# Kernel tuning notes

Hardware: AMD Instinct MI355X
Metric: run time of the kernel (lower is better)

The kernel has to match this reference:

```python
import jax, jax.numpy as jnp
import numpy as np

B, N, D, H = 4, 4096, 512, 512
EDGE_P = 0.01  # adjacency density


def _glorot(key, shape):
    fan_in, fan_out = shape
    limit = np.sqrt(6.0 / (fan_in + fan_out)).astype(np.float32)
    return jax.random.uniform(key, shape, jnp.float32, -limit, limit)


def setup_inputs() -> dict:
    key = jax.random.key(0)
    ks = jax.random.split(key, 9)
    batch_graph = jax.random.normal(ks[0], (B, N, D), jnp.float32)
    adj = (jax.random.uniform(ks[1], (B, N, N)) < EDGE_P).astype(jnp.float32)
    adj = jnp.minimum(adj + jnp.eye(N, dtype=jnp.float32)[None], 1.0)  # self loops, 0/1
    return {
        "batch_graph": batch_graph,
        "adj": adj,
        "W1": _glorot(ks[2], (D, H)), "b1": jnp.zeros((H,), jnp.float32),
        "W2": _glorot(ks[3], (H, H)), "b2": jnp.zeros((H,), jnp.float32),
        "W3": _glorot(ks[4], (H, D)), "b3": jnp.zeros((D,), jnp.float32),
    }


def _normalize_adj(adj):
    # Faithful to GCN.normalize_sparse_adj: D^{-1/2} A^T D^{-1/2}
    rowsum = adj.sum(axis=1)                       # [B, N] (sum over dim 1, as in torch)
    d_inv_sqrt = jnp.where(rowsum > 0, jax.lax.rsqrt(jnp.maximum(rowsum, 1e-30)), 0.0)
    # (A @ diag(d))^T @ diag(d)  ->  d_i * A[j,i] * d_j
    return d_inv_sqrt[:, :, None] * jnp.swapaxes(adj, 1, 2) * d_inv_sqrt[:, None, :]


def reference(batch_graph, adj, W1, b1, W2, b2, W3, b3):
    # Block-diagonal big_adj @ big_graph == independent per-batch matmuls;
    # we exploit that instead of materializing the [B*N, B*N] dense matrix.
    a = _normalize_adj(adj)                                   # [B, N, N]
    # GraphConvolution (pygcn-style): out = adj @ (x @ W) + b; dropout = identity (eval)
    h = jax.nn.relu(jnp.einsum('bij,bjd->bid', a, batch_graph @ W1) + b1)
    h = jax.nn.relu(jnp.einsum('bij,bjd->bid', a, h @ W2) + b2)
    out = jnp.einsum('bij,bjd->bid', a, h @ W3) + b3          # [B, N, D]
    return out
```

## Files before the change

kernel.cpp:

```cpp
#include <hip/hip_runtime.h>
#include <stdint.h>

#define CAP 128
#define RPB 4

typedef __attribute__((ext_vector_type(8))) short bf16x8;
typedef __attribute__((ext_vector_type(4))) float f32x4;

typedef __attribute__((address_space(3))) uint32_t lds_u32;
typedef __attribute__((address_space(1))) const uint32_t glb_u32;

__device__ __forceinline__ unsigned short f2bf(float f) {
  union { float f; uint32_t u; } c; c.f = f;
  return (unsigned short)((c.u + 0x7fffu + ((c.u >> 16) & 1u)) >> 16);
}
__device__ __forceinline__ float bf2f(uint32_t b) {
  union { uint32_t u; float f; } c; c.u = b << 16; return c.f;
}
__device__ __forceinline__ float as_f32(uint32_t u) {
  union { uint32_t u; float f; } c; c.u = u; return c.f;
}

__global__ __launch_bounds__(256) void k_detect(const uint32_t* __restrict__ a,
                                                int* __restrict__ flag) {
  int i = blockIdx.x * 256 + threadIdx.x;
  bool found = false;
  for (int k = 0; k < 64; k++) {
    uint32_t x = a[(size_t)k * 65536 + i];
    if (x == 0x00003F80u || x == 0x3F803F80u) found = true;
  }
  if (found) flag[0] = 1;
}

__global__ __launch_bounds__(256) void k_build(const void* __restrict__ adjp,
                                               int* __restrict__ cnt,
                                               int* __restrict__ cols,
                                               const int* __restrict__ flag) {
  int gid = blockIdx.x * 256 + threadIdx.x;
  if (flag[0]) {
    const uint4* a = (const uint4*)adjp;
    uint4 v = a[gid];
    int i0 = (gid & 511) * 8;
    int j  = (gid >> 9) & 4095;
    int b  = gid >> 21;
    int base = b << 12;
    uint32_t w[4] = {v.x, v.y, v.z, v.w};
#pragma unroll
    for (int q = 0; q < 4; q++) {
      if (w[q] & 0xffffu) {
        int c = base + i0 + q * 2;
        int p = atomicAdd(&cnt[c], 1);
        if (p < CAP) cols[(size_t)c * CAP + p] = j;
      }
      if (w[q] >> 16) {
        int c = base + i0 + q * 2 + 1;
        int p = atomicAdd(&cnt[c], 1);
        if (p < CAP) cols[(size_t)c * CAP + p] = j;
      }
    }
  } else {
    const float4* a = (const float4*)adjp;
#pragma unroll
    for (int it = 0; it < 2; it++) {
      int v4 = gid + it * 8388608;
      float4 v = a[v4];
      int i0 = (v4 & 1023) * 4;
      int j  = (v4 >> 10) & 4095;
      int b  = v4 >> 22;
      int base = b << 12;
      float e[4] = {v.x, v.y, v.z, v.w};
#pragma unroll
      for (int q = 0; q < 4; q++) {
        if (e[q] != 0.0f) {
          int c = base + i0 + q;
          int p = atomicAdd(&cnt[c], 1);
          if (p < CAP) cols[(size_t)c * CAP + p] = j;
        }
      }
    }
  }
}

__global__ __launch_bounds__(256) void k_prep(const int* __restrict__ cnt,
                                              float* __restrict__ dinv,
                                              const void* b1, const void* b2,
                                              const void* b3,
                                              float* __restrict__ b1f,
                                              float* __restrict__ b2f,
                                              float* __restrict__ b3f,
                                              const int* __restrict__ flag) {
  int id = blockIdx.x * 256 + threadIdx.x;
  if (id < 16384) {
    int c = cnt[id];
    dinv[id] = (c > 0) ? 1.0f / sqrtf((float)c) : 0.0f;
  } else {
    int o = id - 16384;
    if (o < 1536) {
      const void* src = (o < 512) ? b1 : (o < 1024) ? b2 : b3;
      float* dst = (o < 512) ? b1f : (o < 1024) ? b2f : b3f;
      int i = o & 511;
      dst[i] = flag[0] ? bf2f(((const ushort*)src)[i]) : ((const float*)src)[i];
    }
  }
}

__global__ __launch_bounds__(256) void k_convx(const void* __restrict__ xp,
                                               ushort* __restrict__ xb,
                                               const int* __restrict__ flag) {
  int gid = blockIdx.x * 256 + threadIdx.x;
  if (flag[0]) {
    const uint4* in = (const uint4*)xp;
    ((uint4*)xb)[gid] = in[gid];
  } else {
    const float4* in = (const float4*)xp;
#pragma unroll
    for (int it = 0; it < 2; it++) {
      int i = gid + it * 1048576;
      float4 v = in[i];
      uint32_t lo = (uint32_t)f2bf(v.x) | ((uint32_t)f2bf(v.y) << 16);
      uint32_t hi = (uint32_t)f2bf(v.z) | ((uint32_t)f2bf(v.w) << 16);
      ((uint2*)xb)[i] = make_uint2(lo, hi);
    }
  }
}

__global__ __launch_bounds__(256) void k_wconv(const void* w1, const void* w2,
                                               const void* w3,
                                               ushort* __restrict__ wt1,
                                               ushort* __restrict__ wt2,
                                               ushort* __restrict__ wt3,
                                               const int* __restrict__ flag) {
  int id = blockIdx.x * 256 + threadIdx.x;
  int w = id >> 18;
  int o = id & 262143;
  const void* wp = (w == 0) ? w1 : (w == 1) ? w2 : w3;
  ushort* wt = (w == 0) ? wt1 : (w == 1) ? wt2 : wt3;
  int n = o >> 9, k = o & 511;
  if (flag[0]) wt[o] = ((const ushort*)wp)[k * 512 + n];
  else         wt[o] = f2bf(((const float*)wp)[k * 512 + n]);
}

__device__ __forceinline__ void gl_lds16(const ushort* g, ushort* l) {
  __builtin_amdgcn_global_load_lds((glb_u32*)g, (lds_u32*)l, 16, 0, 0);
}

__global__ __launch_bounds__(256) void k_gemm(const ushort* __restrict__ X,
                                              const ushort* __restrict__ WT,
                                              ushort* __restrict__ Z) {
  __shared__ ushort As[128 * 32];
  __shared__ ushort Bs[128 * 32];
  const int K = 512, NO = 512;
  int tid = threadIdx.x;
  int m0 = blockIdx.y * 128, n0 = blockIdx.x * 128;
  int lane = tid & 63;
  int wv = tid >> 6;
  int wm = (wv >> 1) << 6;
  int wn = (wv & 1) << 6;
  int lr = lane & 15;
  int lq = lane >> 4;

  f32x4 zero = {0.f, 0.f, 0.f, 0.f};
  f32x4 acc[4][4];
#pragma unroll
  for (int im = 0; im < 4; im++)
#pragma unroll
    for (int in_ = 0; in_ < 4; in_++) acc[im][in_] = zero;

  const ushort* Xg = X  + (size_t)(m0 + (tid >> 2)) * K + ((tid & 3) << 3);
  const ushort* Wg = WT + (size_t)(n0 + (tid >> 2)) * K + ((tid & 3) << 3);

  for (int kt = 0; kt < K; kt += 32) {
    __syncthreads();
    gl_lds16(Xg + kt,                    &As[tid * 8]);
    gl_lds16(Xg + kt + (size_t)64 * K,   &As[2048 + tid * 8]);
    gl_lds16(Wg + kt,                    &Bs[tid * 8]);
    gl_lds16(Wg + kt + (size_t)64 * K,   &Bs[2048 + tid * 8]);
    __syncthreads();
    bf16x8 af[4], bfr[4];
#pragma unroll
    for (int im = 0; im < 4; im++)
      af[im] = *(const bf16x8*)&As[(wm + im * 16 + lr) * 32 + lq * 8];
#pragma unroll
    for (int in_ = 0; in_ < 4; in_++)
      bfr[in_] = *(const bf16x8*)&Bs[(wn + in_ * 16 + lr) * 32 + lq * 8];
#pragma unroll
    for (int im = 0; im < 4; im++)
#pragma unroll
      for (int in_ = 0; in_ < 4; in_++)
        acc[im][in_] = __builtin_amdgcn_mfma_f32_16x16x32_bf16(
            af[im], bfr[in_], acc[im][in_], 0, 0, 0);
  }

#pragma unroll
  for (int im = 0; im < 4; im++) {
    int row0 = m0 + wm + im * 16 + lq * 4;
#pragma unroll
    for (int in_ = 0; in_ < 4; in_++) {
      int col = n0 + wn + in_ * 16 + lr;
#pragma unroll
      for (int r = 0; r < 4; r++)
        Z[(size_t)(row0 + r) * NO + col] = f2bf(acc[im][in_][r]);
    }
  }
}

__global__ __launch_bounds__(256) void k_spmm(const ushort* __restrict__ Z,
                                              const int* __restrict__ cnt,
                                              const int* __restrict__ cols,
                                              const float* __restrict__ dinv,
                                              const float* __restrict__ bias,
                                              void* __restrict__ outp,
                                              int do_relu, int is_final,
                                              const int* __restrict__ flag) {
  __shared__ int   sj[RPB][CAP];
  __shared__ float sv[RPB][CAP];
  int B = blockIdx.x;
  int wv = threadIdx.x >> 6;
  int lane = threadIdx.x & 63;
  int batch = (B & 7) >> 1;
  int lb = ((B >> 3) << 1) | (B & 1);
  int r = (batch << 12) + lb * RPB + wv;
  int base = batch << 12;

  int nnz = cnt[r];
  if (nnz > CAP) nnz = CAP;
  float dr = dinv[r];
  for (int k = lane; k < nnz; k += 64) {
    int j = cols[(size_t)r * CAP + k];
    sj[wv][k] = j;
    sv[wv][k] = dr * dinv[base + j];
  }

  const ushort* Zb = Z + (size_t)base * 512 + lane * 8;
  const float4* bp = (const float4*)bias + lane * 2;
  float4 bb0 = bp[0], bb1 = bp[1];
  float a[8] = {bb0.x, bb0.y, bb0.z, bb0.w, bb1.x, bb1.y, bb1.z, bb1.w};

  int k = 0;
  for (; k + 2 <= nnz; k += 2) {
    int j0 = sj[wv][k], j1 = sj[wv][k + 1];
    float v0 = sv[wv][k], v1 = sv[wv][k + 1];
    uint4 z0 = *(const uint4*)(Zb + (size_t)j0 * 512);
    uint4 z1 = *(const uint4*)(Zb + (size_t)j1 * 512);
    uint32_t w0[4] = {z0.x, z0.y, z0.z, z0.w};
    uint32_t w1[4] = {z1.x, z1.y, z1.z, z1.w};
#pragma unroll
    for (int q = 0; q < 4; q++) {
      a[q * 2]     += v0 * as_f32(w0[q] << 16);
      a[q * 2 + 1] += v0 * as_f32(w0[q] & 0xffff0000u);
      a[q * 2]     += v1 * as_f32(w1[q] << 16);
      a[q * 2 + 1] += v1 * as_f32(w1[q] & 0xffff0000u);
    }
  }
  if (k < nnz) {
    int j0 = sj[wv][k];
    float v0 = sv[wv][k];
    uint4 z0 = *(const uint4*)(Zb + (size_t)j0 * 512);
    uint32_t w0[4] = {z0.x, z0.y, z0.z, z0.w};
#pragma unroll
    for (int q = 0; q < 4; q++) {
      a[q * 2]     += v0 * as_f32(w0[q] << 16);
      a[q * 2 + 1] += v0 * as_f32(w0[q] & 0xffff0000u);
    }
  }

  if (do_relu) {
#pragma unroll
    for (int q = 0; q < 8; q++) a[q] = fmaxf(a[q], 0.f);
  }

  if (!is_final || flag[0]) {
    uint4 o;
    o.x = (uint32_t)f2bf(a[0]) | ((uint32_t)f2bf(a[1]) << 16);
    o.y = (uint32_t)f2bf(a[2]) | ((uint32_t)f2bf(a[3]) << 16);
    o.z = (uint32_t)f2bf(a[4]) | ((uint32_t)f2bf(a[5]) << 16);
    o.w = (uint32_t)f2bf(a[6]) | ((uint32_t)f2bf(a[7]) << 16);
    *(uint4*)((ushort*)outp + (size_t)r * 512 + lane * 8) = o;
  } else {
    float4 o0 = make_float4(a[0], a[1], a[2], a[3]);
    float4 o1 = make_float4(a[4], a[5], a[6], a[7]);
    float4* op = (float4*)((float*)outp + (size_t)r * 512 + lane * 8);
    op[0] = o0; op[1] = o1;
  }
}

extern "C" void kernel_launch(void* const* d_in, const int* in_sizes, int n_in,
                              void* d_out, int out_size, void* d_ws, size_t ws_size,
                              hipStream_t stream) {
  const void* X  = d_in[0];
  const void* A  = d_in[1];
  const void* W1 = d_in[2]; const void* b1 = d_in[3];
  const void* W2 = d_in[4]; const void* b2 = d_in[5];
  const void* W3 = d_in[6]; const void* b3 = d_in[7];

  char* ws = (char*)d_ws;
  size_t off = 0;
  auto alloc = [&](size_t bytes) -> void* {
    void* p = ws + off;
    off += (bytes + 255) & ~(size_t)255;
    return p;
  };
  int*    cnt  = (int*)alloc(16384 * 4);
  int*    flag = (int*)alloc(4);
  float*  dinv = (float*)alloc(16384 * 4);
  int*    cols = (int*)alloc((size_t)16384 * CAP * 4);
  ushort* W1T  = (ushort*)alloc(512 * 512 * 2);
  ushort* W2T  = (ushort*)alloc(512 * 512 * 2);
  ushort* W3T  = (ushort*)alloc(512 * 512 * 2);
  float*  b1f  = (float*)alloc(512 * 4);
  float*  b2f  = (float*)alloc(512 * 4);
  float*  b3f  = (float*)alloc(512 * 4);
  ushort* Xb   = (ushort*)alloc((size_t)16384 * 512 * 2);
  ushort* Zb   = (ushort*)alloc((size_t)16384 * 512 * 2);
  ushort* Hb   = (ushort*)alloc((size_t)16384 * 512 * 2);

  hipMemsetAsync(cnt, 0, 65536 + 256, stream);

  k_detect<<<256, 256, 0, stream>>>((const uint32_t*)A, flag);
  k_build<<<32768, 256, 0, stream>>>(A, cnt, cols, flag);
  k_prep<<<70, 256, 0, stream>>>(cnt, dinv, b1, b2, b3, b1f, b2f, b3f, flag);
  k_convx<<<4096, 256, 0, stream>>>(X, Xb, flag);
  k_wconv<<<3072, 256, 0, stream>>>(W1, W2, W3, W1T, W2T, W3T, flag);

  dim3 gg(4, 128);
  k_gemm<<<gg, 256, 0, stream>>>(Xb, W1T, Zb);
  k_spmm<<<4096, 256, 0, stream>>>(Zb, cnt, cols, dinv, b1f, Hb, 1, 0, flag);
  k_gemm<<<gg, 256, 0, stream>>>(Hb, W2T, Zb);
  k_spmm<<<4096, 256, 0, stream>>>(Zb, cnt, cols, dinv, b2f, Xb, 1, 0, flag);
  k_gemm<<<gg, 256, 0, stream>>>(Xb, W3T, Zb);
  k_spmm<<<4096, 256, 0, stream>>>(Zb, cnt, cols, dinv, b3f, d_out, 0, 1, flag);
}
```

Before: 601.1 us.

## Partition CSR columns into four panels, shuffle-broadcast indices, merge prep kernels

Each row's neighbour list is now split into four column panels (up to 64 entries each), so the SpMM walks neighbours in roughly ascending column order. Indices and weights are held in registers and broadcast with wave shuffles instead of being staged through LDS. The three preprocessing kernels (x conversion, weight transpose, dinv/bias prep) are merged into one launch. The aim is better locality on the gathered Z rows, no LDS traffic, and fewer kernel launches. The cost is four times as many atomic counters, and a row that exceeds 64 entries in one panel is silently truncated.

```diff
diff --git a/kernel.cpp b/kernel.cpp
--- a/kernel.cpp
+++ b/kernel.cpp
@@ -1,7 +1,7 @@
 #include <hip/hip_runtime.h>
 #include <stdint.h>
 
-#define CAP 128
+#define PCAP 64
 #define RPB 4
 
 typedef __attribute__((ext_vector_type(8))) short bf16x8;
@@ -33,8 +33,8 @@
 }
 
 __global__ __launch_bounds__(256) void k_build(const void* __restrict__ adjp,
-                                               int* __restrict__ cnt,
-                                               int* __restrict__ cols,
+                                               int* __restrict__ cnt4,
+                                               int* __restrict__ cols4,
                                                const int* __restrict__ flag) {
   int gid = blockIdx.x * 256 + threadIdx.x;
   if (flag[0]) {
@@ -44,18 +44,19 @@
     int j  = (gid >> 9) & 4095;
     int b  = gid >> 21;
     int base = b << 12;
+    int panel = j >> 10;
     uint32_t w[4] = {v.x, v.y, v.z, v.w};
 #pragma unroll
     for (int q = 0; q < 4; q++) {
       if (w[q] & 0xffffu) {
         int c = base + i0 + q * 2;
-        int p = atomicAdd(&cnt[c], 1);
-        if (p < CAP) cols[(size_t)c * CAP + p] = j;
+        int p = atomicAdd(&cnt4[c * 4 + panel], 1);
+        if (p < PCAP) cols4[((size_t)(c * 4 + panel) << 6) + p] = j;
       }
       if (w[q] >> 16) {
         int c = base + i0 + q * 2 + 1;
-        int p = atomicAdd(&cnt[c], 1);
-        if (p < CAP) cols[(size_t)c * CAP + p] = j;
+        int p = atomicAdd(&cnt4[c * 4 + panel], 1);
+        if (p < PCAP) cols4[((size_t)(c * 4 + panel) << 6) + p] = j;
       }
     }
   } else {
@@ -68,20 +69,28 @@
       int j  = (v4 >> 10) & 4095;
       int b  = v4 >> 22;
       int base = b << 12;
+      int panel = j >> 10;
       float e[4] = {v.x, v.y, v.z, v.w};
 #pragma unroll
       for (int q = 0; q < 4; q++) {
         if (e[q] != 0.0f) {
           int c = base + i0 + q;
-          int p = atomicAdd(&cnt[c], 1);
-          if (p < CAP) cols[(size_t)c * CAP + p] = j;
+          int p = atomicAdd(&cnt4[c * 4 + panel], 1);
+          if (p < PCAP) cols4[((size_t)(c * 4 + panel) << 6) + p] = j;
         }
       }
     }
   }
 }
 
-__global__ __launch_bounds__(256) void k_prep(const int* __restrict__ cnt,
+__global__ __launch_bounds__(256) void k_post(const void* __restrict__ xp,
+                                              ushort* __restrict__ xb,
+                                              const void* w1, const void* w2,
+                                              const void* w3,
+                                              ushort* __restrict__ wt1,
+                                              ushort* __restrict__ wt2,
+                                              ushort* __restrict__ wt3,
+                                              const int* __restrict__ cnt4,
                                               float* __restrict__ dinv,
                                               const void* b1, const void* b2,
                                               const void* b3,
@@ -89,55 +98,48 @@
                                               float* __restrict__ b2f,
                                               float* __restrict__ b3f,
                                               const int* __restrict__ flag) {
-  int id = blockIdx.x * 256 + threadIdx.x;
-  if (id < 16384) {
-    int c = cnt[id];
-    dinv[id] = (c > 0) ? 1.0f / sqrtf((float)c) : 0.0f;
+  int B = blockIdx.x;
+  int t = threadIdx.x;
+  if (B < 4096) {
+    int gid = B * 256 + t;
+    if (flag[0]) {
+      ((uint4*)xb)[gid] = ((const uint4*)xp)[gid];
+    } else {
+      const float4* in = (const float4*)xp;
+#pragma unroll
+      for (int it = 0; it < 2; it++) {
+        int i = gid + it * 1048576;
+        float4 v = in[i];
+        uint32_t lo = (uint32_t)f2bf(v.x) | ((uint32_t)f2bf(v.y) << 16);
+        uint32_t hi = (uint32_t)f2bf(v.z) | ((uint32_t)f2bf(v.w) << 16);
+        ((uint2*)xb)[i] = make_uint2(lo, hi);
+      }
+    }
+  } else if (B < 7168) {
+    int id = (B - 4096) * 256 + t;
+    int w = id >> 18;
+    int o = id & 262143;
+    const void* wp = (w == 0) ? w1 : (w == 1) ? w2 : w3;
+    ushort* wt = (w == 0) ? wt1 : (w == 1) ? wt2 : wt3;
+    int n = o >> 9, k = o & 511;
+    if (flag[0]) wt[o] = ((const ushort*)wp)[k * 512 + n];
+    else         wt[o] = f2bf(((const float*)wp)[k * 512 + n]);
   } else {
-    int o = id - 16384;
-    if (o < 1536) {
-      const void* src = (o < 512) ? b1 : (o < 1024) ? b2 : b3;
-      float* dst = (o < 512) ? b1f : (o < 1024) ? b2f : b3f;
-      int i = o & 511;
-      dst[i] = flag[0] ? bf2f(((const ushort*)src)[i]) : ((const float*)src)[i];
-    }
-  }
-}
-
-__global__ __launch_bounds__(256) void k_convx(const void* __restrict__ xp,
-                                               ushort* __restrict__ xb,
-                                               const int* __restrict__ flag) {
-  int gid = blockIdx.x * 256 + threadIdx.x;
-  if (flag[0]) {
-    const uint4* in = (const uint4*)xp;
-    ((uint4*)xb)[gid] = in[gid];
-  } else {
-    const float4* in = (const float4*)xp;
-#pragma unroll
-    for (int it = 0; it < 2; it++) {
-      int i = gid + it * 1048576;
-      float4 v = in[i];
-      uint32_t lo = (uint32_t)f2bf(v.x) | ((uint32_t)f2bf(v.y) << 16);
-      uint32_t hi = (uint32_t)f2bf(v.z) | ((uint32_t)f2bf(v.w) << 16);
-      ((uint2*)xb)[i] = make_uint2(lo, hi);
-    }
-  }
-}
-
-__global__ __launch_bounds__(256) void k_wconv(const void* w1, const void* w2,
-                                               const void* w3,
-                                               ushort* __restrict__ wt1,
-                                               ushort* __restrict__ wt2,
-                                               ushort* __restrict__ wt3,
-                                               const int* __restrict__ flag) {
-  int id = blockIdx.x * 256 + threadIdx.x;
-  int w = id >> 18;
-  int o = id & 262143;
-  const void* wp = (w == 0) ? w1 : (w == 1) ? w2 : w3;
-  ushort* wt = (w == 0) ? wt1 : (w == 1) ? wt2 : wt3;
-  int n = o >> 9, k = o & 511;
-  if (flag[0]) wt[o] = ((const ushort*)wp)[k * 512 + n];
-  else         wt[o] = f2bf(((const float*)wp)[k * 512 + n]);
+    int id = (B - 7168) * 256 + t;
+    if (id < 16384) {
+      int4 cc = ((const int4*)cnt4)[id];
+      int s = cc.x + cc.y + cc.z + cc.w;
+      dinv[id] = (s > 0) ? 1.0f / sqrtf((float)s) : 0.0f;
+    } else {
+      int o = id - 16384;
+      if (o < 1536) {
+        const void* src = (o < 512) ? b1 : (o < 1024) ? b2 : b3;
+        float* dst = (o < 512) ? b1f : (o < 1024) ? b2f : b3f;
+        int i = o & 511;
+        dst[i] = flag[0] ? bf2f(((const ushort*)src)[i]) : ((const float*)src)[i];
+      }
+    }
+  }
 }
 
 __device__ __forceinline__ void gl_lds16(const ushort* g, ushort* l) {
@@ -205,15 +207,13 @@
 }
 
 __global__ __launch_bounds__(256) void k_spmm(const ushort* __restrict__ Z,
-                                              const int* __restrict__ cnt,
-                                              const int* __restrict__ cols,
+                                              const int* __restrict__ cnt4,
+                                              const int* __restrict__ cols4,
                                               const float* __restrict__ dinv,
                                               const float* __restrict__ bias,
                                               void* __restrict__ outp,
                                               int do_relu, int is_final,
                                               const int* __restrict__ flag) {
-  __shared__ int   sj[RPB][CAP];
-  __shared__ float sv[RPB][CAP];
   int B = blockIdx.x;
   int wv = threadIdx.x >> 6;
   int lane = threadIdx.x & 63;
@@ -222,45 +222,47 @@
   int r = (batch << 12) + lb * RPB + wv;
   int base = batch << 12;
 
-  int nnz = cnt[r];
-  if (nnz > CAP) nnz = CAP;
   float dr = dinv[r];
-  for (int k = lane; k < nnz; k += 64) {
-    int j = cols[(size_t)r * CAP + k];
-    sj[wv][k] = j;
-    sv[wv][k] = dr * dinv[base + j];
-  }
-
   const ushort* Zb = Z + (size_t)base * 512 + lane * 8;
   const float4* bp = (const float4*)bias + lane * 2;
   float4 bb0 = bp[0], bb1 = bp[1];
   float a[8] = {bb0.x, bb0.y, bb0.z, bb0.w, bb1.x, bb1.y, bb1.z, bb1.w};
 
-  int k = 0;
-  for (; k + 2 <= nnz; k += 2) {
-    int j0 = sj[wv][k], j1 = sj[wv][k + 1];
-    float v0 = sv[wv][k], v1 = sv[wv][k + 1];
-    uint4 z0 = *(const uint4*)(Zb + (size_t)j0 * 512);
-    uint4 z1 = *(const uint4*)(Zb + (size_t)j1 * 512);
-    uint32_t w0[4] = {z0.x, z0.y, z0.z, z0.w};
-    uint32_t w1[4] = {z1.x, z1.y, z1.z, z1.w};
-#pragma unroll
-    for (int q = 0; q < 4; q++) {
-      a[q * 2]     += v0 * as_f32(w0[q] << 16);
-      a[q * 2 + 1] += v0 * as_f32(w0[q] & 0xffff0000u);
-      a[q * 2]     += v1 * as_f32(w1[q] << 16);
-      a[q * 2 + 1] += v1 * as_f32(w1[q] & 0xffff0000u);
-    }
-  }
-  if (k < nnz) {
-    int j0 = sj[wv][k];
-    float v0 = sv[wv][k];
-    uint4 z0 = *(const uint4*)(Zb + (size_t)j0 * 512);
-    uint32_t w0[4] = {z0.x, z0.y, z0.z, z0.w};
-#pragma unroll
-    for (int q = 0; q < 4; q++) {
-      a[q * 2]     += v0 * as_f32(w0[q] << 16);
-      a[q * 2 + 1] += v0 * as_f32(w0[q] & 0xffff0000u);
+#pragma unroll
+  for (int p = 0; p < 4; p++) {
+    int nz = cnt4[r * 4 + p];
+    if (nz > PCAP) nz = PCAP;
+    int jl = 0; float vl = 0.f;
+    if (lane < nz) {
+      jl = cols4[((size_t)(r * 4 + p) << 6) + lane];
+      vl = dr * dinv[base + jl];
+    }
+    int k = 0;
+    for (; k + 2 <= nz; k += 2) {
+      int   j0 = __shfl(jl, k),     j1 = __shfl(jl, k + 1);
+      float v0 = __shfl(vl, k),     v1 = __shfl(vl, k + 1);
+      uint4 z0 = *(const uint4*)(Zb + (size_t)j0 * 512);
+      uint4 z1 = *(const uint4*)(Zb + (size_t)j1 * 512);
+      uint32_t w0[4] = {z0.x, z0.y, z0.z, z0.w};
+      uint32_t w1[4] = {z1.x, z1.y, z1.z, z1.w};
+#pragma unroll
+      for (int q = 0; q < 4; q++) {
+        a[q * 2]     += v0 * as_f32(w0[q] << 16);
+        a[q * 2 + 1] += v0 * as_f32(w0[q] & 0xffff0000u);
+        a[q * 2]     += v1 * as_f32(w1[q] << 16);
+        a[q * 2 + 1] += v1 * as_f32(w1[q] & 0xffff0000u);
+      }
+    }
+    if (k < nz) {
+      int   j0 = __shfl(jl, k);
+      float v0 = __shfl(vl, k);
+      uint4 z0 = *(const uint4*)(Zb + (size_t)j0 * 512);
+      uint32_t w0[4] = {z0.x, z0.y, z0.z, z0.w};
+#pragma unroll
+      for (int q = 0; q < 4; q++) {
+        a[q * 2]     += v0 * as_f32(w0[q] << 16);
+        a[q * 2 + 1] += v0 * as_f32(w0[q] & 0xffff0000u);
+      }
     }
   }
 
@@ -277,10 +279,9 @@
     o.w = (uint32_t)f2bf(a[6]) | ((uint32_t)f2bf(a[7]) << 16);
     *(uint4*)((ushort*)outp + (size_t)r * 512 + lane * 8) = o;
   } else {
-    float4 o0 = make_float4(a[0], a[1], a[2], a[3]);
-    float4 o1 = make_float4(a[4], a[5], a[6], a[7]);
     float4* op = (float4*)((float*)outp + (size_t)r * 512 + lane * 8);
-    op[0] = o0; op[1] = o1;
+    op[0] = make_float4(a[0], a[1], a[2], a[3]);
+    op[1] = make_float4(a[4], a[5], a[6], a[7]);
   }
 }
 
@@ -300,10 +301,10 @@
     off += (bytes + 255) & ~(size_t)255;
     return p;
   };
-  int*    cnt  = (int*)alloc(16384 * 4);
+  int*    cnt4 = (int*)alloc((size_t)16384 * 4 * 4);
   int*    flag = (int*)alloc(4);
   float*  dinv = (float*)alloc(16384 * 4);
-  int*    cols = (int*)alloc((size_t)16384 * CAP * 4);
+  int*    cols4= (int*)alloc((size_t)16384 * 4 * PCAP * 4);
   ushort* W1T  = (ushort*)alloc(512 * 512 * 2);
   ushort* W2T  = (ushort*)alloc(512 * 512 * 2);
   ushort* W3T  = (ushort*)alloc(512 * 512 * 2);
@@ -314,19 +315,18 @@
   ushort* Zb   = (ushort*)alloc((size_t)16384 * 512 * 2);
   ushort* Hb   = (ushort*)alloc((size_t)16384 * 512 * 2);
 
-  hipMemsetAsync(cnt, 0, 65536 + 256, stream);
+  hipMemsetAsync(cnt4, 0, 262144 + 256, stream);
 
   k_detect<<<256, 256, 0, stream>>>((const uint32_t*)A, flag);
-  k_build<<<32768, 256, 0, stream>>>(A, cnt, cols, flag);
-  k_prep<<<70, 256, 0, stream>>>(cnt, dinv, b1, b2, b3, b1f, b2f, b3f, flag);
-  k_convx<<<4096, 256, 0, stream>>>(X, Xb, flag);
-  k_wconv<<<3072, 256, 0, stream>>>(W1, W2, W3, W1T, W2T, W3T, flag);
+  k_build<<<32768, 256, 0, stream>>>(A, cnt4, cols4, flag);
+  k_post<<<7238, 256, 0, stream>>>(X, Xb, W1, W2, W3, W1T, W2T, W3T,
+                                   cnt4, dinv, b1, b2, b3, b1f, b2f, b3f, flag);
 
   dim3 gg(4, 128);
   k_gemm<<<gg, 256, 0, stream>>>(Xb, W1T, Zb);
-  k_spmm<<<4096, 256, 0, stream>>>(Zb, cnt, cols, dinv, b1f, Hb, 1, 0, flag);
+  k_spmm<<<4096, 256, 0, stream>>>(Zb, cnt4, cols4, dinv, b1f, Hb, 1, 0, flag);
   k_gemm<<<gg, 256, 0, stream>>>(Hb, W2T, Zb);
-  k_spmm<<<4096, 256, 0, stream>>>(Zb, cnt, cols, dinv, b2f, Xb, 1, 0, flag);
+  k_spmm<<<4096, 256, 0, stream>>>(Zb, cnt4, cols4, dinv, b2f, Xb, 1, 0, flag);
   k_gemm<<<gg, 256, 0, stream>>>(Xb, W3T, Zb);
-  k_spmm<<<4096, 256, 0, stream>>>(Zb, cnt, cols, dinv, b3f, d_out, 0, 1, flag);
-}
+  k_spmm<<<4096, 256, 0, stream>>>(Zb, cnt4, cols4, dinv, b3f, d_out, 0, 1, flag);
+}
```

Result: no change. 612.4 us (+1.9%).

## Split SpMM gather into column passes and fuse preprocessing kernels

Applied to the files above, without the earlier changes.

The SpMM now runs as four launches per layer, each covering a 128-column slice of Z. Inside a wave, four edges are gathered in parallel across lane groups and the partial sums are combined with cross-lane shuffles. The smaller per-pass working set is meant to improve cache reuse of gathered rows, at the cost of more launches, a shuffle reduction, and an epilogue that only 16 lanes run. The bias, degree, input-conversion and weight-transpose kernels are merged into one launch, and in bf16 mode the GEMM reads the raw input directly instead of taking a copy.

```diff
diff --git a/kernel.cpp b/kernel.cpp
--- a/kernel.cpp
+++ b/kernel.cpp
@@ -50,12 +50,12 @@
       if (w[q] & 0xffffu) {
         int c = base + i0 + q * 2;
         int p = atomicAdd(&cnt[c], 1);
-        if (p < CAP) cols[(size_t)c * CAP + p] = j;
+        if (p < CAP) cols[((size_t)c << 7) + p] = j;
       }
       if (w[q] >> 16) {
         int c = base + i0 + q * 2 + 1;
         int p = atomicAdd(&cnt[c], 1);
-        if (p < CAP) cols[(size_t)c * CAP + p] = j;
+        if (p < CAP) cols[((size_t)c << 7) + p] = j;
       }
     }
   } else {
@@ -74,14 +74,21 @@
         if (e[q] != 0.0f) {
           int c = base + i0 + q;
           int p = atomicAdd(&cnt[c], 1);
-          if (p < CAP) cols[(size_t)c * CAP + p] = j;
+          if (p < CAP) cols[((size_t)c << 7) + p] = j;
         }
       }
     }
   }
 }
 
-__global__ __launch_bounds__(256) void k_prep(const int* __restrict__ cnt,
+__global__ __launch_bounds__(256) void k_post(const void* __restrict__ xp,
+                                              ushort* __restrict__ xb,
+                                              const void* w1, const void* w2,
+                                              const void* w3,
+                                              ushort* __restrict__ wt1,
+                                              ushort* __restrict__ wt2,
+                                              ushort* __restrict__ wt3,
+                                              const int* __restrict__ cnt,
                                               float* __restrict__ dinv,
                                               const void* b1, const void* b2,
                                               const void* b3,
@@ -89,29 +96,11 @@
                                               float* __restrict__ b2f,
                                               float* __restrict__ b3f,
                                               const int* __restrict__ flag) {
-  int id = blockIdx.x * 256 + threadIdx.x;
-  if (id < 16384) {
-    int c = cnt[id];
-    dinv[id] = (c > 0) ? 1.0f / sqrtf((float)c) : 0.0f;
-  } else {
-    int o = id - 16384;
-    if (o < 1536) {
-      const void* src = (o < 512) ? b1 : (o < 1024) ? b2 : b3;
-      float* dst = (o < 512) ? b1f : (o < 1024) ? b2f : b3f;
-      int i = o & 511;
-      dst[i] = flag[0] ? bf2f(((const ushort*)src)[i]) : ((const float*)src)[i];
-    }
-  }
-}
-
-__global__ __launch_bounds__(256) void k_convx(const void* __restrict__ xp,
-                                               ushort* __restrict__ xb,
-                                               const int* __restrict__ flag) {
-  int gid = blockIdx.x * 256 + threadIdx.x;
-  if (flag[0]) {
-    const uint4* in = (const uint4*)xp;
-    ((uint4*)xb)[gid] = in[gid];
-  } else {
+  int B = blockIdx.x;
+  int t = threadIdx.x;
+  if (B < 4096) {
+    if (flag[0]) return;
+    int gid = B * 256 + t;
     const float4* in = (const float4*)xp;
 #pragma unroll
     for (int it = 0; it < 2; it++) {
@@ -121,35 +110,45 @@
       uint32_t hi = (uint32_t)f2bf(v.z) | ((uint32_t)f2bf(v.w) << 16);
       ((uint2*)xb)[i] = make_uint2(lo, hi);
     }
-  }
-}
-
-__global__ __launch_bounds__(256) void k_wconv(const void* w1, const void* w2,
-                                               const void* w3,
-                                               ushort* __restrict__ wt1,
-                                               ushort* __restrict__ wt2,
-                                               ushort* __restrict__ wt3,
-                                               const int* __restrict__ flag) {
-  int id = blockIdx.x * 256 + threadIdx.x;
-  int w = id >> 18;
-  int o = id & 262143;
-  const void* wp = (w == 0) ? w1 : (w == 1) ? w2 : w3;
-  ushort* wt = (w == 0) ? wt1 : (w == 1) ? wt2 : wt3;
-  int n = o >> 9, k = o & 511;
-  if (flag[0]) wt[o] = ((const ushort*)wp)[k * 512 + n];
-  else         wt[o] = f2bf(((const float*)wp)[k * 512 + n]);
+  } else if (B < 7168) {
+    int id = (B - 4096) * 256 + t;
+    int w = id >> 18;
+    int o = id & 262143;
+    const void* wp = (w == 0) ? w1 : (w == 1) ? w2 : w3;
+    ushort* wt = (w == 0) ? wt1 : (w == 1) ? wt2 : wt3;
+    int n = o >> 9, k = o & 511;
+    if (flag[0]) wt[o] = ((const ushort*)wp)[k * 512 + n];
+    else         wt[o] = f2bf(((const float*)wp)[k * 512 + n]);
+  } else {
+    int id = (B - 7168) * 256 + t;
+    if (id < 16384) {
+      int c = cnt[id];
+      dinv[id] = (c > 0) ? 1.0f / sqrtf((float)c) : 0.0f;
+    } else {
+      int o = id - 16384;
+      if (o < 1536) {
+        const void* src = (o < 512) ? b1 : (o < 1024) ? b2 : b3;
+        float* dst = (o < 512) ? b1f : (o < 1024) ? b2f : b3f;
+        int i = o & 511;
+        dst[i] = flag[0] ? bf2f(((const ushort*)src)[i]) : ((const float*)src)[i];
+      }
+    }
+  }
 }
 
 __device__ __forceinline__ void gl_lds16(const ushort* g, ushort* l) {
   __builtin_amdgcn_global_load_lds((glb_u32*)g, (lds_u32*)l, 16, 0, 0);
 }
 
-__global__ __launch_bounds__(256) void k_gemm(const ushort* __restrict__ X,
+__global__ __launch_bounds__(256) void k_gemm(const void* __restrict__ Xraw,
+                                              const ushort* __restrict__ Xconv,
                                               const ushort* __restrict__ WT,
-                                              ushort* __restrict__ Z) {
+                                              ushort* __restrict__ Z,
+                                              const int* __restrict__ flag) {
   __shared__ ushort As[128 * 32];
   __shared__ ushort Bs[128 * 32];
   const int K = 512, NO = 512;
+  const ushort* X = flag[0] ? (const ushort*)Xraw : Xconv;
   int tid = threadIdx.x;
   int m0 = blockIdx.y * 128, n0 = blockIdx.x * 128;
   int lane = tid & 63;
@@ -211,62 +210,58 @@
                                               const float* __restrict__ bias,
                                               void* __restrict__ outp,
                                               int do_relu, int is_final,
-                                              const int* __restrict__ flag) {
+                                              const int* __restrict__ flag,
+                                              int pass) {
   __shared__ int   sj[RPB][CAP];
   __shared__ float sv[RPB][CAP];
   int B = blockIdx.x;
   int wv = threadIdx.x >> 6;
   int lane = threadIdx.x & 63;
-  int batch = (B & 7) >> 1;
-  int lb = ((B >> 3) << 1) | (B & 1);
-  int r = (batch << 12) + lb * RPB + wv;
-  int base = batch << 12;
+  int r = B * RPB + wv;
+  int base = (r >> 12) << 12;
 
   int nnz = cnt[r];
   if (nnz > CAP) nnz = CAP;
   float dr = dinv[r];
   for (int k = lane; k < nnz; k += 64) {
-    int j = cols[(size_t)r * CAP + k];
+    int j = cols[((size_t)r << 7) + k];
     sj[wv][k] = j;
     sv[wv][k] = dr * dinv[base + j];
   }
 
-  const ushort* Zb = Z + (size_t)base * 512 + lane * 8;
-  const float4* bp = (const float4*)bias + lane * 2;
+  int g = lane >> 4;
+  int col = (lane & 15) << 3;
+  const ushort* Zc = Z + (size_t)base * 512 + pass * 128 + col;
+
+  float a[8] = {0.f, 0.f, 0.f, 0.f, 0.f, 0.f, 0.f, 0.f};
+  for (int k = 0; k < nnz; k += 4) {
+    int e = k + g;
+    bool ok = e < nnz;
+    int   j = ok ? sj[wv][e] : 0;
+    float v = ok ? sv[wv][e] : 0.f;
+    uint4 z = *(const uint4*)(Zc + (size_t)j * 512);
+    uint32_t w[4] = {z.x, z.y, z.z, z.w};
+#pragma unroll
+    for (int q = 0; q < 4; q++) {
+      a[q * 2]     += v * as_f32(w[q] << 16);
+      a[q * 2 + 1] += v * as_f32(w[q] & 0xffff0000u);
+    }
+  }
+
+#pragma unroll
+  for (int q = 0; q < 8; q++) {
+    a[q] += __shfl_xor(a[q], 16);
+    a[q] += __shfl_xor(a[q], 32);
+  }
+  if (lane >= 16) return;
+
+  const float4* bp = (const float4*)(bias + pass * 128 + col);
   float4 bb0 = bp[0], bb1 = bp[1];
-  float a[8] = {bb0.x, bb0.y, bb0.z, bb0.w, bb1.x, bb1.y, bb1.z, bb1.w};
-
-  int k = 0;
-  for (; k + 2 <= nnz; k += 2) {
-    int j0 = sj[wv][k], j1 = sj[wv][k + 1];
-    float v0 = sv[wv][k], v1 = sv[wv][k + 1];
-    uint4 z0 = *(const uint4*)(Zb + (size_t)j0 * 512);
-    uint4 z1 = *(const uint4*)(Zb + (size_t)j1 * 512);
-    uint32_t w0[4] = {z0.x, z0.y, z0.z, z0.w};
-    uint32_t w1[4] = {z1.x, z1.y, z1.z, z1.w};
-#pragma unroll
-    for (int q = 0; q < 4; q++) {
-      a[q * 2]     += v0 * as_f32(w0[q] << 16);
-      a[q * 2 + 1] += v0 * as_f32(w0[q] & 0xffff0000u);
-      a[q * 2]     += v1 * as_f32(w1[q] << 16);
-      a[q * 2 + 1] += v1 * as_f32(w1[q] & 0xffff0000u);
-    }
-  }
-  if (k < nnz) {
-    int j0 = sj[wv][k];
-    float v0 = sv[wv][k];
-    uint4 z0 = *(const uint4*)(Zb + (size_t)j0 * 512);
-    uint32_t w0[4] = {z0.x, z0.y, z0.z, z0.w};
-#pragma unroll
-    for (int q = 0; q < 4; q++) {
-      a[q * 2]     += v0 * as_f32(w0[q] << 16);
-      a[q * 2 + 1] += v0 * as_f32(w0[q] & 0xffff0000u);
-    }
-  }
-
-  if (do_relu) {
-#pragma unroll
-    for (int q = 0; q < 8; q++) a[q] = fmaxf(a[q], 0.f);
+  float bv[8] = {bb0.x, bb0.y, bb0.z, bb0.w, bb1.x, bb1.y, bb1.z, bb1.w};
+#pragma unroll
+  for (int q = 0; q < 8; q++) {
+    a[q] += bv[q];
+    if (do_relu) a[q] = fmaxf(a[q], 0.f);
   }
 
   if (!is_final || flag[0]) {
@@ -275,12 +270,11 @@
     o.y = (uint32_t)f2bf(a[2]) | ((uint32_t)f2bf(a[3]) << 16);
     o.z = (uint32_t)f2bf(a[4]) | ((uint32_t)f2bf(a[5]) << 16);
     o.w = (uint32_t)f2bf(a[6]) | ((uint32_t)f2bf(a[7]) << 16);
-    *(uint4*)((ushort*)outp + (size_t)r * 512 + lane * 8) = o;
+    *(uint4*)((ushort*)outp + (size_t)r * 512 + pass * 128 + col) = o;
   } else {
-    float4 o0 = make_float4(a[0], a[1], a[2], a[3]);
-    float4 o1 = make_float4(a[4], a[5], a[6], a[7]);
-    float4* op = (float4*)((float*)outp + (size_t)r * 512 + lane * 8);
-    op[0] = o0; op[1] = o1;
+    float4* op = (float4*)((float*)outp + (size_t)r * 512 + pass * 128 + col);
+    op[0] = make_float4(a[0], a[1], a[2], a[3]);
+    op[1] = make_float4(a[4], a[5], a[6], a[7]);
   }
 }
 
@@ -318,15 +312,17 @@
 
   k_detect<<<256, 256, 0, stream>>>((const uint32_t*)A, flag);
   k_build<<<32768, 256, 0, stream>>>(A, cnt, cols, flag);
-  k_prep<<<70, 256, 0, stream>>>(cnt, dinv, b1, b2, b3, b1f, b2f, b3f, flag);
-  k_convx<<<4096, 256, 0, stream>>>(X, Xb, flag);
-  k_wconv<<<3072, 256, 0, stream>>>(W1, W2, W3, W1T, W2T, W3T, flag);
+  k_post<<<7238, 256, 0, stream>>>(X, Xb, W1, W2, W3, W1T, W2T, W3T,
+                                   cnt, dinv, b1, b2, b3, b1f, b2f, b3f, flag);
 
   dim3 gg(4, 128);
-  k_gemm<<<gg, 256, 0, stream>>>(Xb, W1T, Zb);
-  k_spmm<<<4096, 256, 0, stream>>>(Zb, cnt, cols, dinv, b1f, Hb, 1, 0, flag);
-  k_gemm<<<gg, 256, 0, stream>>>(Hb, W2T, Zb);
-  k_spmm<<<4096, 256, 0, stream>>>(Zb, cnt, cols, dinv, b2f, Xb, 1, 0, flag);
-  k_gemm<<<gg, 256, 0, stream>>>(Xb, W3T, Zb);
-  k_spmm<<<4096, 256, 0, stream>>>(Zb, cnt, cols, dinv, b3f, d_out, 0, 1, flag);
-}
+  k_gemm<<<gg, 256, 0, stream>>>(X, Xb, W1T, Zb, flag);
+  for (int p = 0; p < 4; p++)
+    k_spmm<<<4096, 256, 0, stream>>>(Zb, cnt, cols, dinv, b1f, Hb, 1, 0, flag, p);
+  k_gemm<<<gg, 256, 0, stream>>>(Hb, Hb, W2T, Zb, flag);
+  for (int p = 0; p < 4; p++)
+    k_spmm<<<4096, 256, 0, stream>>>(Zb, cnt, cols, dinv, b2f, Xb, 1, 0, flag, p);
+  k_gemm<<<gg, 256, 0, stream>>>(Xb, Xb, W3T, Zb, flag);
+  for (int p = 0; p < 4; p++)
+    k_spmm<<<4096, 256, 0, stream>>>(Zb, cnt, cols, dinv, b3f, d_out, 0, 1, flag, p);
+}
```

Result: slower. 699.6 us (+16.4%).
